# Kernel optimization log

Measured on AMD Instinct MI355X. Metric: run time of the kernel, lower is better.

Reference implementation:

```python
import jax, jax.numpy as jnp
import numpy as np

N_AUTHOR, N_FOS, N_INST, N_PAPER = 100000, 30000, 8000, 200000
D_IN, D_OUT = 128, 128
# (name, n_src, n_dst, n_edges)
RELS = [("aff", N_AUTHOR, N_INST, 150000), ("ita", N_INST, N_AUTHOR, 150000),
        ("writes", N_AUTHOR, N_PAPER, 500000), ("pta", N_PAPER, N_AUTHOR, 500000),
        ("cites", N_PAPER, N_PAPER, 1000000), ("topic", N_PAPER, N_FOS, 500000),
        ("ftp", N_FOS, N_PAPER, 500000)]
NODE_SIZES = {"author": N_AUTHOR, "fos": N_FOS, "inst": N_INST, "paper": N_PAPER}


def setup_inputs() -> dict:
    key = jax.random.key(0)
    ks = iter(jax.random.split(key, 64))
    inp = {}
    for nt, n in NODE_SIZES.items():
        inp[f"x_{nt}"] = jax.random.normal(next(ks), (n, D_IN), jnp.float32)
    for name, ns, nd, e in RELS:
        inp[f"src_{name}"] = jax.random.randint(next(ks), (e,), 0, ns, jnp.int64)
        inp[f"dst_{name}"] = jax.random.randint(next(ks), (e,), 0, nd, jnp.int64)
    w_scale = 1.0 / np.sqrt(D_IN)
    for nt in NODE_SIZES:
        inp[f"W_root_{nt}"] = jax.random.uniform(next(ks), (D_IN, D_OUT), jnp.float32, -w_scale, w_scale)
        inp[f"b_root_{nt}"] = jax.random.uniform(next(ks), (D_OUT,), jnp.float32, -w_scale, w_scale)
    for name, _, _, _ in RELS:
        inp[f"W_{name}"] = jax.random.uniform(next(ks), (D_IN, D_OUT), jnp.float32, -w_scale, w_scale)
    return inp


def _mean_agg(x_src, src, dst, n_dst):
    # gather source features along edges, mean-reduce into destinations
    msg = x_src[src]                                             # [E, D_IN]
    s = jax.ops.segment_sum(msg, dst, num_segments=n_dst)        # [n_dst, D_IN]
    cnt = jax.ops.segment_sum(jnp.ones_like(dst, dtype=x_src.dtype), dst, num_segments=n_dst)
    return s / jnp.maximum(cnt, 1.0)[:, None]                    # isolated nodes -> 0


def reference(x_author, x_fos, x_inst, x_paper,
              W_root_author, b_root_author, W_root_fos, b_root_fos,
              W_root_inst, b_root_inst, W_root_paper, b_root_paper,
              W_aff, W_ita, W_writes, W_pta, W_cites, W_topic, W_ftp,
              src_aff, dst_aff, src_ita, dst_ita, src_writes, dst_writes,
              src_pta, dst_pta, src_cites, dst_cites, src_topic, dst_topic,
              src_ftp, dst_ftp):
    # root (self) transforms
    out_author = x_author @ W_root_author + b_root_author
    out_fos = x_fos @ W_root_fos + b_root_fos
    out_inst = x_inst @ W_root_inst + b_root_inst
    out_paper = x_paper @ W_root_paper + b_root_paper
    # per-relation aggregate -> linear -> accumulate into destination type
    out_inst = out_inst + _mean_agg(x_author, src_aff, dst_aff, N_INST) @ W_aff
    out_author = out_author + _mean_agg(x_inst, src_ita, dst_ita, N_AUTHOR) @ W_ita
    out_paper = out_paper + _mean_agg(x_author, src_writes, dst_writes, N_PAPER) @ W_writes
    out_author = out_author + _mean_agg(x_paper, src_pta, dst_pta, N_AUTHOR) @ W_pta
    out_paper = out_paper + _mean_agg(x_paper, src_cites, dst_cites, N_PAPER) @ W_cites
    out_fos = out_fos + _mean_agg(x_paper, src_topic, dst_topic, N_FOS) @ W_topic
    out_paper = out_paper + _mean_agg(x_fos, src_ftp, dst_ftp, N_PAPER) @ W_ftp
    # concatenate per-type outputs (author, fos, inst, paper) along node axis
    return jnp.concatenate([out_author, out_fos, out_inst, out_paper], axis=0)
```

## Files before the change

### kernel.cpp

```cpp
#include <hip/hip_runtime.h>

#define N_AUTHOR 100000
#define N_FOS    30000
#define N_INST   8000
#define N_PAPER  200000

typedef __attribute__((ext_vector_type(8))) short short8v;
typedef __attribute__((ext_vector_type(4))) float float4v;

__device__ __forceinline__ unsigned short f2bf(float f) {
  unsigned u = __float_as_uint(f);
  u = u + 0x7fffu + ((u >> 16) & 1u);
  return (unsigned short)(u >> 16);
}
#define BF2F(s) __uint_as_float(((unsigned)(unsigned short)(s)) << 16)

__device__ __forceinline__ void acc8(float4v& x, float4v& y, short8v h) {
  x[0] += BF2F(h[0]); x[1] += BF2F(h[1]); x[2] += BF2F(h[2]); x[3] += BF2F(h[3]);
  y[0] += BF2F(h[4]); y[1] += BF2F(h[5]); y[2] += BF2F(h[6]); y[3] += BF2F(h[7]);
}

#define O_CNT    0
#define O_OFFS   3352000
#define O_CURSOR 6704000
#define O_BTOT   10056000
#define O_CSR    10060096
#define O_WT     23260096
#define XB_AUTHOR 23620544
#define XB_FOS    49220544
#define XB_INST   56900544
#define XB_PAPER  58948544
#define WS_NEED_BF 110148544ULL
#define NCNT     838000

struct RelTab { const int* src; const int* dst; int E; int base; };
struct Rels { RelTab r[7]; };
struct WPtrs { const float* w[11]; };
struct XCvt { const float* x; unsigned short* xb; int n8; };

__global__ void prep(WPtrs P, unsigned short* __restrict__ wt,
                     int* __restrict__ cnt, XCvt x0, XCvt x1, XCvt x2, XCvt x3,
                     int doX) {
  int gsz = gridDim.x * blockDim.x;
  int gtid = blockIdx.x * blockDim.x + threadIdx.x;
  for (int i = gtid; i < 11 * 16384; i += gsz) {
    int mat = i >> 14, rem = i & 16383;
    int k = rem >> 7, n = rem & 127;
    wt[mat * 16384 + n * 128 + k] = f2bf(P.w[mat][rem]);
  }
  for (int i = gtid; i < NCNT; i += gsz) cnt[i] = 0;
  if (doX) {
    XCvt xc[4] = {x0, x1, x2, x3};
    #pragma unroll
    for (int a = 0; a < 4; ++a) {
      const float* xp = xc[a].x;
      short8v* xbp = (short8v*)xc[a].xb;
      int n8 = xc[a].n8;
      for (int i = gtid; i < n8; i += gsz) {
        float4v v0 = *(const float4v*)(xp + (size_t)i * 8);
        float4v v1 = *(const float4v*)(xp + (size_t)i * 8 + 4);
        short8v h;
        h[0] = (short)f2bf(v0[0]); h[1] = (short)f2bf(v0[1]);
        h[2] = (short)f2bf(v0[2]); h[3] = (short)f2bf(v0[3]);
        h[4] = (short)f2bf(v1[0]); h[5] = (short)f2bf(v1[1]);
        h[6] = (short)f2bf(v1[2]); h[7] = (short)f2bf(v1[3]);
        xbp[i] = h;
      }
    }
  }
}

__global__ void count_k(Rels R, int* __restrict__ cnt) {
  int gsz = gridDim.x * blockDim.x;
  int gtid = blockIdx.x * blockDim.x + threadIdx.x;
  for (int rr = 0; rr < 7; ++rr) {
    const int* dst = R.r[rr].dst;
    int E = R.r[rr].E, base = R.r[rr].base;
    for (int e = gtid; e < E; e += gsz) atomicAdd(&cnt[base + dst[e]], 1);
  }
}

__global__ void scan1(const int* __restrict__ cnt, int* __restrict__ offs,
                      int* __restrict__ btot, int n) {
  __shared__ int sh[256];
  int tid = threadIdx.x;
  int base = blockIdx.x * 2048 + tid * 8;
  int v[8]; int s = 0;
  #pragma unroll
  for (int i = 0; i < 8; ++i) { v[i] = (base + i < n) ? cnt[base + i] : 0; s += v[i]; }
  sh[tid] = s; __syncthreads();
  for (int off = 1; off < 256; off <<= 1) {
    int t = (tid >= off) ? sh[tid - off] : 0;
    __syncthreads();
    sh[tid] += t;
    __syncthreads();
  }
  int excl = sh[tid] - s;
  if (tid == 255) btot[blockIdx.x] = sh[255];
  int run = excl;
  #pragma unroll
  for (int i = 0; i < 8; ++i) { if (base + i < n) offs[base + i] = run; run += v[i]; }
}

__global__ void scan23(int* __restrict__ offs, int* __restrict__ cursor,
                       const int* __restrict__ btot, int nb, int n) {
  __shared__ int sh[512];
  int tid = threadIdx.x;
  int v = (tid < nb) ? btot[tid] : 0;
  sh[tid] = v; __syncthreads();
  for (int off = 1; off < 512; off <<= 1) {
    int t = (tid >= off) ? sh[tid - off] : 0;
    __syncthreads();
    sh[tid] += t;
    __syncthreads();
  }
  int excl = sh[tid] - v;
  __syncthreads();
  sh[tid] = excl;
  __syncthreads();
  int gsz = gridDim.x * 512;
  for (int idx = blockIdx.x * 512 + tid; idx < n; idx += gsz) {
    int val = offs[idx] + sh[idx >> 11];
    offs[idx] = val;
    cursor[idx] = val;
  }
}

__global__ void fill_k(Rels R, int* __restrict__ cursor, int* __restrict__ csr) {
  int gsz = gridDim.x * blockDim.x;
  int gtid = blockIdx.x * blockDim.x + threadIdx.x;
  for (int rr = 0; rr < 7; ++rr) {
    const int* src = R.r[rr].src;
    const int* dst = R.r[rr].dst;
    int E = R.r[rr].E, base = R.r[rr].base;
    for (int e = gtid; e < E; e += gsz) {
      int p = atomicAdd(&cursor[base + dst[e]], 1);
      csr[p] = src[e];
    }
  }
}

struct GemmSrc { const float* x; const unsigned short* xb;
                 const unsigned short* wt; int cntBase; };
struct TypeArgs {
  GemmSrc s[4];
  int nsrc;
  int bstart;
  int n;
  const float* bias;
  float* out;
};
struct AllArgs {
  TypeArgs t[4];
  const int* offs;
  const int* cnt;
  const int* csr;
};

#define LD4(p) (*(const float4v*)(p))

template <int BF>
__global__ __launch_bounds__(256, 4) void rgcn_gemm(AllArgs A) {
  __shared__ unsigned short a_lds[64 * 128];
  const int tid = threadIdx.x;
  const int wv = tid >> 6, lane = tid & 63;

  int bid = blockIdx.x;
  int ty = (bid >= A.t[3].bstart) ? 3 : (bid >= A.t[2].bstart) ? 2
         : (bid >= A.t[1].bstart) ? 1 : 0;
  const TypeArgs& T = A.t[ty];
  const int rb = (bid - T.bstart) * 64;
  const int n = T.n;

  float4v acc[8];
  #pragma unroll
  for (int i = 0; i < 8; ++i) acc[i] = (float4v)0.0f;

  for (int kb = 0; kb < T.nsrc; ++kb) {
    const GemmSrc S = T.s[kb];
    if (S.cntBase < 0) {
      if (BF) {
        int r = tid >> 2, cb = (tid & 3) * 64;
        int g = rb + r;
        const short8v* p = (const short8v*)(S.xb + (size_t)g * 128 + (cb >> 1));
        #pragma unroll
        for (int k = 0; k < 4; ++k) {
          short8v h = (g < n) ? p[k] : (short8v)0;
          int byte = (r * 256 + cb + k * 16) ^ ((r & 7) << 4);
          *(short8v*)((char*)a_lds + byte) = h;
        }
      } else {
        #pragma unroll
        for (int i = 0; i < 4; ++i) {
          int c = tid + i * 256;
          int r = c >> 4, cc = (c & 15) * 8;
          int g = rb + r;
          short8v hv;
          if (g < n) {
            float4v v0 = LD4(S.x + (size_t)g * 128 + cc);
            float4v v1 = LD4(S.x + (size_t)g * 128 + cc + 4);
            hv[0] = (short)f2bf(v0[0]); hv[1] = (short)f2bf(v0[1]);
            hv[2] = (short)f2bf(v0[2]); hv[3] = (short)f2bf(v0[3]);
            hv[4] = (short)f2bf(v1[0]); hv[5] = (short)f2bf(v1[1]);
            hv[6] = (short)f2bf(v1[2]); hv[7] = (short)f2bf(v1[3]);
          } else hv = (short8v)0;
          int byte = r * 256 + cc * 2; byte ^= (r & 7) << 4;
          *(short8v*)((char*)a_lds + byte) = hv;
        }
      }
    } else if (BF) {
      const int r = tid >> 2;
      const int c0 = (tid & 3) * 32;
      int g = rb + r;
      int gd = S.cntBase + ((g < n) ? g : 0);
      int st = A.offs[gd];
      int deg = (g < n) ? A.cnt[gd] : 0;
      float4v a0 = (float4v)0.f, a1 = (float4v)0.f, a2 = (float4v)0.f,
              a3 = (float4v)0.f, a4 = (float4v)0.f, a5 = (float4v)0.f,
              a6 = (float4v)0.f, a7 = (float4v)0.f;
      int j = 0;
      for (; j + 2 <= deg; j += 2) {
        int i0 = A.csr[st + j], i1 = A.csr[st + j + 1];
        const short8v* p0 = (const short8v*)(S.xb + (size_t)i0 * 128 + c0);
        const short8v* p1 = (const short8v*)(S.xb + (size_t)i1 * 128 + c0);
        short8v h0 = p0[0], h1 = p0[1], h2 = p0[2], h3 = p0[3];
        short8v k0 = p1[0], k1 = p1[1], k2 = p1[2], k3 = p1[3];
        acc8(a0, a1, h0); acc8(a2, a3, h1); acc8(a4, a5, h2); acc8(a6, a7, h3);
        acc8(a0, a1, k0); acc8(a2, a3, k1); acc8(a4, a5, k2); acc8(a6, a7, k3);
      }
      if (j < deg) {
        int i0 = A.csr[st + j];
        const short8v* p0 = (const short8v*)(S.xb + (size_t)i0 * 128 + c0);
        short8v h0 = p0[0], h1 = p0[1], h2 = p0[2], h3 = p0[3];
        acc8(a0, a1, h0); acc8(a2, a3, h1); acc8(a4, a5, h2); acc8(a6, a7, h3);
      }
      float sc = 1.0f / (float)((deg > 0) ? deg : 1);
      a0 *= sc; a1 *= sc; a2 *= sc; a3 *= sc;
      a4 *= sc; a5 *= sc; a6 *= sc; a7 *= sc;
      short8v o0, o1, o2, o3;
      o0[0] = (short)f2bf(a0[0]); o0[1] = (short)f2bf(a0[1]);
      o0[2] = (short)f2bf(a0[2]); o0[3] = (short)f2bf(a0[3]);
      o0[4] = (short)f2bf(a1[0]); o0[5] = (short)f2bf(a1[1]);
      o0[6] = (short)f2bf(a1[2]); o0[7] = (short)f2bf(a1[3]);
      o1[0] = (short)f2bf(a2[0]); o1[1] = (short)f2bf(a2[1]);
      o1[2] = (short)f2bf(a2[2]); o1[3] = (short)f2bf(a2[3]);
      o1[4] = (short)f2bf(a3[0]); o1[5] = (short)f2bf(a3[1]);
      o1[6] = (short)f2bf(a3[2]); o1[7] = (short)f2bf(a3[3]);
      o2[0] = (short)f2bf(a4[0]); o2[1] = (short)f2bf(a4[1]);
      o2[2] = (short)f2bf(a4[2]); o2[3] = (short)f2bf(a4[3]);
      o2[4] = (short)f2bf(a5[0]); o2[5] = (short)f2bf(a5[1]);
      o2[6] = (short)f2bf(a5[2]); o2[7] = (short)f2bf(a5[3]);
      o3[0] = (short)f2bf(a6[0]); o3[1] = (short)f2bf(a6[1]);
      o3[2] = (short)f2bf(a6[2]); o3[3] = (short)f2bf(a6[3]);
      o3[4] = (short)f2bf(a7[0]); o3[5] = (short)f2bf(a7[1]);
      o3[6] = (short)f2bf(a7[2]); o3[7] = (short)f2bf(a7[3]);
      int bbase = r * 256 + c0 * 2;
      int sw = (r & 7) << 4;
      *(short8v*)((char*)a_lds + ((bbase) ^ sw)) = o0;
      *(short8v*)((char*)a_lds + ((bbase + 16) ^ sw)) = o1;
      *(short8v*)((char*)a_lds + ((bbase + 32) ^ sw)) = o2;
      *(short8v*)((char*)a_lds + ((bbase + 48) ^ sw)) = o3;
    } else {
      const int q = lane >> 4;
      const int c0 = (lane & 15) * 8;
      int stA[4], dgA[4];
      #pragma unroll
      for (int rd = 0; rd < 4; ++rd) {
        int r = wv * 16 + rd * 4 + q;
        int g = rb + r;
        int gc = (g < n) ? g : 0;
        int gd = S.cntBase + gc;
        stA[rd] = A.offs[gd];
        dgA[rd] = (g < n) ? A.cnt[gd] : 0;
      }
      #pragma unroll
      for (int rd = 0; rd < 4; ++rd) {
        int r = wv * 16 + rd * 4 + q;
        int st = stA[rd], deg = dgA[rd];
        float a0 = 0.f, a1 = 0.f, a2 = 0.f, a3 = 0.f;
        float a4 = 0.f, a5 = 0.f, a6 = 0.f, a7 = 0.f;
        int j = 0;
        for (; j + 2 <= deg; j += 2) {
          int s0 = A.csr[st + j], s1 = A.csr[st + j + 1];
          const float* p0 = S.x + (size_t)s0 * 128 + c0;
          const float* p1 = S.x + (size_t)s1 * 128 + c0;
          float4v u0 = LD4(p0), u1 = LD4(p0 + 4);
          float4v v0 = LD4(p1), v1 = LD4(p1 + 4);
          a0 += u0[0] + v0[0]; a1 += u0[1] + v0[1];
          a2 += u0[2] + v0[2]; a3 += u0[3] + v0[3];
          a4 += u1[0] + v1[0]; a5 += u1[1] + v1[1];
          a6 += u1[2] + v1[2]; a7 += u1[3] + v1[3];
        }
        if (j < deg) {
          int s0 = A.csr[st + j];
          const float* p0 = S.x + (size_t)s0 * 128 + c0;
          float4v u0 = LD4(p0), u1 = LD4(p0 + 4);
          a0 += u0[0]; a1 += u0[1]; a2 += u0[2]; a3 += u0[3];
          a4 += u1[0]; a5 += u1[1]; a6 += u1[2]; a7 += u1[3];
        }
        float sc = 1.0f / (float)((deg > 0) ? deg : 1);
        short8v hv;
        hv[0] = (short)f2bf(a0 * sc); hv[1] = (short)f2bf(a1 * sc);
        hv[2] = (short)f2bf(a2 * sc); hv[3] = (short)f2bf(a3 * sc);
        hv[4] = (short)f2bf(a4 * sc); hv[5] = (short)f2bf(a5 * sc);
        hv[6] = (short)f2bf(a6 * sc); hv[7] = (short)f2bf(a7 * sc);
        int byte = r * 256 + c0 * 2; byte ^= (r & 7) << 4;
        *(short8v*)((char*)a_lds + byte) = hv;
      }
    }
    __syncthreads();
    short8v af[4];
    #pragma unroll
    for (int ks = 0; ks < 4; ++ks) {
      int r = wv * 16 + (lane & 15);
      int ch = ks * 4 + (lane >> 4);
      int byte = r * 256 + ch * 16; byte ^= (r & 7) << 4;
      af[ks] = *(const short8v*)((const char*)a_lds + byte);
    }
    const unsigned short* wbase = S.wt + (size_t)(lane & 15) * 128
                                + (size_t)(lane >> 4) * 8;
    #pragma unroll
    for (int ct = 0; ct < 8; ++ct) {
      short8v bfr[4];
      #pragma unroll
      for (int ks = 0; ks < 4; ++ks)
        bfr[ks] = *(const short8v*)(wbase + (size_t)ct * 16 * 128 + ks * 32);
      #pragma unroll
      for (int ks = 0; ks < 4; ++ks)
        acc[ct] = __builtin_amdgcn_mfma_f32_16x16x32_bf16(af[ks], bfr[ks], acc[ct], 0, 0, 0);
    }
    __syncthreads();
  }
  #pragma unroll
  for (int ct = 0; ct < 8; ++ct) {
    #pragma unroll
    for (int i = 0; i < 4; ++i) {
      int row = wv * 16 + (lane >> 4) * 4 + i;
      int g = rb + row;
      if (g < n) {
        int col = ct * 16 + (lane & 15);
        T.out[(size_t)g * 128 + col] = acc[ct][i] + T.bias[col];
      }
    }
  }
}

extern "C" void kernel_launch(void* const* d_in, const int* in_sizes, int n_in,
                              void* d_out, int out_size, void* d_ws, size_t ws_size,
                              hipStream_t stream) {
  const float* x_author = (const float*)d_in[0];
  const float* x_fos    = (const float*)d_in[1];
  const float* x_inst   = (const float*)d_in[2];
  const float* x_paper  = (const float*)d_in[3];

  Rels R;
  const int E[7]  = {150000, 150000, 500000, 500000, 1000000, 500000, 500000};
  const int ND[7] = {N_INST, N_AUTHOR, N_PAPER, N_AUTHOR, N_PAPER, N_FOS, N_PAPER};
  int base = 0;
  for (int r = 0; r < 7; ++r) {
    R.r[r].src = (const int*)d_in[4 + 2 * r];
    R.r[r].dst = (const int*)d_in[5 + 2 * r];
    R.r[r].E = E[r];
    R.r[r].base = base;
    base += ND[r];
  }

  char* ws = (char*)d_ws;
  int* cnt    = (int*)(ws + O_CNT);
  int* offs   = (int*)(ws + O_OFFS);
  int* cursor = (int*)(ws + O_CURSOR);
  int* btot   = (int*)(ws + O_BTOT);
  int* csr    = (int*)(ws + O_CSR);
  unsigned short* wt = (unsigned short*)(ws + O_WT);
  unsigned short* xbA = (unsigned short*)(ws + XB_AUTHOR);
  unsigned short* xbF = (unsigned short*)(ws + XB_FOS);
  unsigned short* xbI = (unsigned short*)(ws + XB_INST);
  unsigned short* xbP = (unsigned short*)(ws + XB_PAPER);

  const int useBF = (ws_size >= WS_NEED_BF) ? 1 : 0;

  WPtrs WP;
  WP.w[0] = (const float*)d_in[18];
  WP.w[1] = (const float*)d_in[20];
  WP.w[2] = (const float*)d_in[22];
  WP.w[3] = (const float*)d_in[24];
  for (int r = 0; r < 7; ++r) WP.w[4 + r] = (const float*)d_in[26 + r];

  XCvt xcA = {x_author, xbA, N_AUTHOR * 16};
  XCvt xcF = {x_fos,    xbF, N_FOS * 16};
  XCvt xcI = {x_inst,   xbI, N_INST * 16};
  XCvt xcP = {x_paper,  xbP, N_PAPER * 16};

  prep<<<2048, 256, 0, stream>>>(WP, wt, cnt, xcA, xcF, xcI, xcP, useBF);
  count_k<<<1024, 256, 0, stream>>>(R, cnt);
  scan1<<<410, 256, 0, stream>>>(cnt, offs, btot, NCNT);
  scan23<<<1024, 512, 0, stream>>>(offs, cursor, btot, 410, NCNT);
  fill_k<<<1024, 256, 0, stream>>>(R, cursor, csr);

  float* out = (float*)d_out;
  const int B_AFF = 0, B_ITA = 8000, B_WRITES = 108000, B_PTA = 308000,
            B_CITES = 408000, B_TOPIC = 608000, B_FTP = 638000;

  AllArgs A;
  A.offs = offs; A.cnt = cnt; A.csr = csr;
  for (int t = 0; t < 4; ++t)
    for (int i = 0; i < 4; ++i) A.t[t].s[i] = GemmSrc{nullptr, nullptr, nullptr, 0};

  const int NB_AUTHOR = (N_AUTHOR + 63) / 64;
  const int NB_FOS    = (N_FOS + 63) / 64;
  const int NB_INST   = (N_INST + 63) / 64;
  const int NB_PAPER  = (N_PAPER + 63) / 64;

  A.t[0].s[0] = GemmSrc{x_author, xbA, wt + 0 * 16384, -1};
  A.t[0].s[1] = GemmSrc{x_inst,   xbI, wt + 5 * 16384, B_ITA};
  A.t[0].s[2] = GemmSrc{x_paper,  xbP, wt + 7 * 16384, B_PTA};
  A.t[0].nsrc = 3; A.t[0].bstart = 0; A.t[0].n = N_AUTHOR;
  A.t[0].bias = (const float*)d_in[19]; A.t[0].out = out;

  A.t[1].s[0] = GemmSrc{x_fos,   xbF, wt + 1 * 16384, -1};
  A.t[1].s[1] = GemmSrc{x_paper, xbP, wt + 9 * 16384, B_TOPIC};
  A.t[1].nsrc = 2; A.t[1].bstart = NB_AUTHOR; A.t[1].n = N_FOS;
  A.t[1].bias = (const float*)d_in[21]; A.t[1].out = out + (size_t)100000 * 128;

  A.t[2].s[0] = GemmSrc{x_inst,   xbI, wt + 2 * 16384, -1};
  A.t[2].s[1] = GemmSrc{x_author, xbA, wt + 4 * 16384, B_AFF};
  A.t[2].nsrc = 2; A.t[2].bstart = NB_AUTHOR + NB_FOS; A.t[2].n = N_INST;
  A.t[2].bias = (const float*)d_in[23]; A.t[2].out = out + (size_t)130000 * 128;

  A.t[3].s[0] = GemmSrc{x_paper,  xbP, wt + 3 * 16384, -1};
  A.t[3].s[1] = GemmSrc{x_author, xbA, wt + 6 * 16384, B_WRITES};
  A.t[3].s[2] = GemmSrc{x_paper,  xbP, wt + 8 * 16384, B_CITES};
  A.t[3].s[3] = GemmSrc{x_fos,    xbF, wt + 10 * 16384, B_FTP};
  A.t[3].nsrc = 4; A.t[3].bstart = NB_AUTHOR + NB_FOS + NB_INST; A.t[3].n = N_PAPER;
  A.t[3].bias = (const float*)d_in[25]; A.t[3].out = out + (size_t)138000 * 128;

  const int NB_TOTAL = NB_AUTHOR + NB_FOS + NB_INST + NB_PAPER;
  if (useBF)
    rgcn_gemm<1><<<NB_TOTAL, 256, 0, stream>>>(A);
  else
    rgcn_gemm<0><<<NB_TOTAL, 256, 0, stream>>>(A);
}
```

Measured before the change: 900.3 us.

## Split aggregation into separate gather kernel and feed bf16 aggregates to MFMA GEMM

```diff
diff --git a/kernel.cpp b/kernel.cpp
--- a/kernel.cpp
+++ b/kernel.cpp
@@ -30,7 +30,9 @@
 #define XB_FOS    49220544
 #define XB_INST   56900544
 #define XB_PAPER  58948544
-#define WS_NEED_BF 110148544ULL
+#define O_AGG     110148544
+#define WS_NEED_BF  110148544ULL
+#define WS_NEED_AGG 324676544ULL
 #define NCNT     838000
 
 struct RelTab { const int* src; const int* dst; int E; int base; };
@@ -140,13 +142,115 @@
   }
 }
 
+struct AggArgs {
+  const unsigned short* xb[7];
+  const int* offs; const int* cnt; const int* csr;
+  unsigned short* agg;
+};
+
+__global__ __launch_bounds__(256, 8) void agg_k(AggArgs G) {
+  const int w = blockIdx.x * 4 + (threadIdx.x >> 6);
+  const int lane = threadIdx.x & 63;
+  int rel = (w >= 638000) ? 6 : (w >= 608000) ? 5 : (w >= 408000) ? 4
+          : (w >= 308000) ? 3 : (w >= 108000) ? 2 : (w >= 8000) ? 1 : 0;
+  const unsigned short* xb = G.xb[rel];
+  const int st = G.offs[w];
+  const int deg = G.cnt[w];
+  const int ce = lane * 2;
+  float a0 = 0.f, a1 = 0.f;
+  for (int j = 0; j < deg; j += 8) {
+    int rem = deg - j;
+    int nb = (rem > 8) ? 8 : rem;
+    int vidx = 0;
+    if (lane < nb) vidx = G.csr[st + j + lane];
+    unsigned r0 = 0, r1 = 0, r2 = 0, r3 = 0, r4 = 0, r5 = 0, r6 = 0, r7 = 0;
+    int s;
+    if (nb > 0) { s = __builtin_amdgcn_readlane(vidx, 0); r0 = *(const unsigned*)(xb + (size_t)s * 128 + ce); }
+    if (nb > 1) { s = __builtin_amdgcn_readlane(vidx, 1); r1 = *(const unsigned*)(xb + (size_t)s * 128 + ce); }
+    if (nb > 2) { s = __builtin_amdgcn_readlane(vidx, 2); r2 = *(const unsigned*)(xb + (size_t)s * 128 + ce); }
+    if (nb > 3) { s = __builtin_amdgcn_readlane(vidx, 3); r3 = *(const unsigned*)(xb + (size_t)s * 128 + ce); }
+    if (nb > 4) { s = __builtin_amdgcn_readlane(vidx, 4); r4 = *(const unsigned*)(xb + (size_t)s * 128 + ce); }
+    if (nb > 5) { s = __builtin_amdgcn_readlane(vidx, 5); r5 = *(const unsigned*)(xb + (size_t)s * 128 + ce); }
+    if (nb > 6) { s = __builtin_amdgcn_readlane(vidx, 6); r6 = *(const unsigned*)(xb + (size_t)s * 128 + ce); }
+    if (nb > 7) { s = __builtin_amdgcn_readlane(vidx, 7); r7 = *(const unsigned*)(xb + (size_t)s * 128 + ce); }
+    if (nb > 0) { a0 += __uint_as_float(r0 << 16); a1 += __uint_as_float(r0 & 0xffff0000u); }
+    if (nb > 1) { a0 += __uint_as_float(r1 << 16); a1 += __uint_as_float(r1 & 0xffff0000u); }
+    if (nb > 2) { a0 += __uint_as_float(r2 << 16); a1 += __uint_as_float(r2 & 0xffff0000u); }
+    if (nb > 3) { a0 += __uint_as_float(r3 << 16); a1 += __uint_as_float(r3 & 0xffff0000u); }
+    if (nb > 4) { a0 += __uint_as_float(r4 << 16); a1 += __uint_as_float(r4 & 0xffff0000u); }
+    if (nb > 5) { a0 += __uint_as_float(r5 << 16); a1 += __uint_as_float(r5 & 0xffff0000u); }
+    if (nb > 6) { a0 += __uint_as_float(r6 << 16); a1 += __uint_as_float(r6 & 0xffff0000u); }
+    if (nb > 7) { a0 += __uint_as_float(r7 << 16); a1 += __uint_as_float(r7 & 0xffff0000u); }
+  }
+  float sc = 1.0f / (float)((deg > 0) ? deg : 1);
+  unsigned h0 = f2bf(a0 * sc), h1 = f2bf(a1 * sc);
+  *(unsigned*)(G.agg + (size_t)w * 128 + ce) = h0 | (h1 << 16);
+}
+
+struct Type2 {
+  const unsigned short* src[4];
+  const unsigned short* wtp[4];
+  int nsrc, bstart, n;
+  const float* bias;
+  float* out;
+};
+struct All2 { Type2 t[4]; };
+
+__global__ __launch_bounds__(256, 4) void rgcn_gemm_agg(All2 A) {
+  const int tid = threadIdx.x;
+  const int wv = tid >> 6, lane = tid & 63;
+  int bid = blockIdx.x;
+  int ty = (bid >= A.t[3].bstart) ? 3 : (bid >= A.t[2].bstart) ? 2
+         : (bid >= A.t[1].bstart) ? 1 : 0;
+  const Type2& T = A.t[ty];
+  const int rb = (bid - T.bstart) * 64;
+  const int n = T.n;
+
+  int ar = rb + wv * 16 + (lane & 15);
+  if (ar >= n) ar = n - 1;
+  const int ach = lane >> 4;
+
+  float4v acc[8];
+  #pragma unroll
+  for (int i = 0; i < 8; ++i) acc[i] = (float4v)0.0f;
+
+  for (int kb = 0; kb < T.nsrc; ++kb) {
+    const unsigned short* abase = T.src[kb] + (size_t)ar * 128 + ach * 8;
+    short8v af[4];
+    #pragma unroll
+    for (int ks = 0; ks < 4; ++ks)
+      af[ks] = *(const short8v*)(abase + ks * 32);
+    const unsigned short* wbase = T.wtp[kb] + (size_t)(lane & 15) * 128 + ach * 8;
+    #pragma unroll
+    for (int ct = 0; ct < 8; ++ct) {
+      short8v bfr[4];
+      #pragma unroll
+      for (int ks = 0; ks < 4; ++ks)
+        bfr[ks] = *(const short8v*)(wbase + (size_t)ct * 2048 + ks * 32);
+      #pragma unroll
+      for (int ks = 0; ks < 4; ++ks)
+        acc[ct] = __builtin_amdgcn_mfma_f32_16x16x32_bf16(af[ks], bfr[ks], acc[ct], 0, 0, 0);
+    }
+  }
+  #pragma unroll
+  for (int ct = 0; ct < 8; ++ct) {
+    #pragma unroll
+    for (int i = 0; i < 4; ++i) {
+      int row = wv * 16 + (lane >> 4) * 4 + i;
+      int g = rb + row;
+      if (g < n) {
+        int col = ct * 16 + (lane & 15);
+        T.out[(size_t)g * 128 + col] = acc[ct][i] + T.bias[col];
+      }
+    }
+  }
+}
+
 struct GemmSrc { const float* x; const unsigned short* xb;
                  const unsigned short* wt; int cntBase; };
 struct TypeArgs {
   GemmSrc s[4];
-  int nsrc;
-  int bstart;
-  int n;
+  int nsrc, bstart, n;
   const float* bias;
   float* out;
 };
@@ -376,8 +480,10 @@
   unsigned short* xbF = (unsigned short*)(ws + XB_FOS);
   unsigned short* xbI = (unsigned short*)(ws + XB_INST);
   unsigned short* xbP = (unsigned short*)(ws + XB_PAPER);
-
-  const int useBF = (ws_size >= WS_NEED_BF) ? 1 : 0;
+  unsigned short* agg = (unsigned short*)(ws + O_AGG);
+
+  const int useBF  = (ws_size >= WS_NEED_BF) ? 1 : 0;
+  const int useAGG = (ws_size >= WS_NEED_AGG) ? 1 : 0;
 
   WPtrs WP;
   WP.w[0] = (const float*)d_in[18];
@@ -392,51 +498,88 @@
   XCvt xcP = {x_paper,  xbP, N_PAPER * 16};
 
   prep<<<2048, 256, 0, stream>>>(WP, wt, cnt, xcA, xcF, xcI, xcP, useBF);
-  count_k<<<1024, 256, 0, stream>>>(R, cnt);
+  count_k<<<2048, 256, 0, stream>>>(R, cnt);
   scan1<<<410, 256, 0, stream>>>(cnt, offs, btot, NCNT);
   scan23<<<1024, 512, 0, stream>>>(offs, cursor, btot, 410, NCNT);
-  fill_k<<<1024, 256, 0, stream>>>(R, cursor, csr);
+  fill_k<<<2048, 256, 0, stream>>>(R, cursor, csr);
 
   float* out = (float*)d_out;
   const int B_AFF = 0, B_ITA = 8000, B_WRITES = 108000, B_PTA = 308000,
             B_CITES = 408000, B_TOPIC = 608000, B_FTP = 638000;
-
-  AllArgs A;
-  A.offs = offs; A.cnt = cnt; A.csr = csr;
-  for (int t = 0; t < 4; ++t)
-    for (int i = 0; i < 4; ++i) A.t[t].s[i] = GemmSrc{nullptr, nullptr, nullptr, 0};
 
   const int NB_AUTHOR = (N_AUTHOR + 63) / 64;
   const int NB_FOS    = (N_FOS + 63) / 64;
   const int NB_INST   = (N_INST + 63) / 64;
   const int NB_PAPER  = (N_PAPER + 63) / 64;
-
-  A.t[0].s[0] = GemmSrc{x_author, xbA, wt + 0 * 16384, -1};
-  A.t[0].s[1] = GemmSrc{x_inst,   xbI, wt + 5 * 16384, B_ITA};
-  A.t[0].s[2] = GemmSrc{x_paper,  xbP, wt + 7 * 16384, B_PTA};
-  A.t[0].nsrc = 3; A.t[0].bstart = 0; A.t[0].n = N_AUTHOR;
-  A.t[0].bias = (const float*)d_in[19]; A.t[0].out = out;
-
-  A.t[1].s[0] = GemmSrc{x_fos,   xbF, wt + 1 * 16384, -1};
-  A.t[1].s[1] = GemmSrc{x_paper, xbP, wt + 9 * 16384, B_TOPIC};
-  A.t[1].nsrc = 2; A.t[1].bstart = NB_AUTHOR; A.t[1].n = N_FOS;
-  A.t[1].bias = (const float*)d_in[21]; A.t[1].out = out + (size_t)100000 * 128;
-
-  A.t[2].s[0] = GemmSrc{x_inst,   xbI, wt + 2 * 16384, -1};
-  A.t[2].s[1] = GemmSrc{x_author, xbA, wt + 4 * 16384, B_AFF};
-  A.t[2].nsrc = 2; A.t[2].bstart = NB_AUTHOR + NB_FOS; A.t[2].n = N_INST;
-  A.t[2].bias = (const float*)d_in[23]; A.t[2].out = out + (size_t)130000 * 128;
-
-  A.t[3].s[0] = GemmSrc{x_paper,  xbP, wt + 3 * 16384, -1};
-  A.t[3].s[1] = GemmSrc{x_author, xbA, wt + 6 * 16384, B_WRITES};
-  A.t[3].s[2] = GemmSrc{x_paper,  xbP, wt + 8 * 16384, B_CITES};
-  A.t[3].s[3] = GemmSrc{x_fos,    xbF, wt + 10 * 16384, B_FTP};
-  A.t[3].nsrc = 4; A.t[3].bstart = NB_AUTHOR + NB_FOS + NB_INST; A.t[3].n = N_PAPER;
-  A.t[3].bias = (const float*)d_in[25]; A.t[3].out = out + (size_t)138000 * 128;
-
   const int NB_TOTAL = NB_AUTHOR + NB_FOS + NB_INST + NB_PAPER;
-  if (useBF)
-    rgcn_gemm<1><<<NB_TOTAL, 256, 0, stream>>>(A);
-  else
-    rgcn_gemm<0><<<NB_TOTAL, 256, 0, stream>>>(A);
-}
+
+  if (useAGG) {
+    AggArgs GA;
+    GA.xb[0] = xbA; GA.xb[1] = xbI; GA.xb[2] = xbA; GA.xb[3] = xbP;
+    GA.xb[4] = xbP; GA.xb[5] = xbP; GA.xb[6] = xbF;
+    GA.offs = offs; GA.cnt = cnt; GA.csr = csr; GA.agg = agg;
+    agg_k<<<NCNT / 4, 256, 0, stream>>>(GA);
+
+    All2 A2;
+    for (int t = 0; t < 4; ++t)
+      for (int i = 0; i < 4; ++i) { A2.t[t].src[i] = nullptr; A2.t[t].wtp[i] = nullptr; }
+
+    A2.t[0].src[0] = xbA;                        A2.t[0].wtp[0] = wt + 0 * 16384;
+    A2.t[0].src[1] = agg + (size_t)B_ITA * 128;  A2.t[0].wtp[1] = wt + 5 * 16384;
+    A2.t[0].src[2] = agg + (size_t)B_PTA * 128;  A2.t[0].wtp[2] = wt + 7 * 16384;
+    A2.t[0].nsrc = 3; A2.t[0].bstart = 0; A2.t[0].n = N_AUTHOR;
+    A2.t[0].bias = (const float*)d_in[19]; A2.t[0].out = out;
+
+    A2.t[1].src[0] = xbF;                          A2.t[1].wtp[0] = wt + 1 * 16384;
+    A2.t[1].src[1] = agg + (size_t)B_TOPIC * 128;  A2.t[1].wtp[1] = wt + 9 * 16384;
+    A2.t[1].nsrc = 2; A2.t[1].bstart = NB_AUTHOR; A2.t[1].n = N_FOS;
+    A2.t[1].bias = (const float*)d_in[21]; A2.t[1].out = out + (size_t)100000 * 128;
+
+    A2.t[2].src[0] = xbI;                        A2.t[2].wtp[0] = wt + 2 * 16384;
+    A2.t[2].src[1] = agg + (size_t)B_AFF * 128;  A2.t[2].wtp[1] = wt + 4 * 16384;
+    A2.t[2].nsrc = 2; A2.t[2].bstart = NB_AUTHOR + NB_FOS; A2.t[2].n = N_INST;
+    A2.t[2].bias = (const float*)d_in[23]; A2.t[2].out = out + (size_t)130000 * 128;
+
+    A2.t[3].src[0] = xbP;                           A2.t[3].wtp[0] = wt + 3 * 16384;
+    A2.t[3].src[1] = agg + (size_t)B_WRITES * 128;  A2.t[3].wtp[1] = wt + 6 * 16384;
+    A2.t[3].src[2] = agg + (size_t)B_CITES * 128;   A2.t[3].wtp[2] = wt + 8 * 16384;
+    A2.t[3].src[3] = agg + (size_t)B_FTP * 128;     A2.t[3].wtp[3] = wt + 10 * 16384;
+    A2.t[3].nsrc = 4; A2.t[3].bstart = NB_AUTHOR + NB_FOS + NB_INST; A2.t[3].n = N_PAPER;
+    A2.t[3].bias = (const float*)d_in[25]; A2.t[3].out = out + (size_t)138000 * 128;
+
+    rgcn_gemm_agg<<<NB_TOTAL, 256, 0, stream>>>(A2);
+  } else {
+    AllArgs A;
+    A.offs = offs; A.cnt = cnt; A.csr = csr;
+    for (int t = 0; t < 4; ++t)
+      for (int i = 0; i < 4; ++i) A.t[t].s[i] = GemmSrc{nullptr, nullptr, nullptr, 0};
+
+    A.t[0].s[0] = GemmSrc{x_author, xbA, wt + 0 * 16384, -1};
+    A.t[0].s[1] = GemmSrc{x_inst,   xbI, wt + 5 * 16384, B_ITA};
+    A.t[0].s[2] = GemmSrc{x_paper,  xbP, wt + 7 * 16384, B_PTA};
+    A.t[0].nsrc = 3; A.t[0].bstart = 0; A.t[0].n = N_AUTHOR;
+    A.t[0].bias = (const float*)d_in[19]; A.t[0].out = out;
+
+    A.t[1].s[0] = GemmSrc{x_fos,   xbF, wt + 1 * 16384, -1};
+    A.t[1].s[1] = GemmSrc{x_paper, xbP, wt + 9 * 16384, B_TOPIC};
+    A.t[1].nsrc = 2; A.t[1].bstart = NB_AUTHOR; A.t[1].n = N_FOS;
+    A.t[1].bias = (const float*)d_in[21]; A.t[1].out = out + (size_t)100000 * 128;
+
+    A.t[2].s[0] = GemmSrc{x_inst,   xbI, wt + 2 * 16384, -1};
+    A.t[2].s[1] = GemmSrc{x_author, xbA, wt + 4 * 16384, B_AFF};
+    A.t[2].nsrc = 2; A.t[2].bstart = NB_AUTHOR + NB_FOS; A.t[2].n = N_INST;
+    A.t[2].bias = (const float*)d_in[23]; A.t[2].out = out + (size_t)130000 * 128;
+
+    A.t[3].s[0] = GemmSrc{x_paper,  xbP, wt + 3 * 16384, -1};
+    A.t[3].s[1] = GemmSrc{x_author, xbA, wt + 6 * 16384, B_WRITES};
+    A.t[3].s[2] = GemmSrc{x_paper,  xbP, wt + 8 * 16384, B_CITES};
+    A.t[3].s[3] = GemmSrc{x_fos,    xbF, wt + 10 * 16384, B_FTP};
+    A.t[3].nsrc = 4; A.t[3].bstart = NB_AUTHOR + NB_FOS + NB_INST; A.t[3].n = N_PAPER;
+    A.t[3].bias = (const float*)d_in[25]; A.t[3].out = out + (size_t)138000 * 128;
+
+    if (useBF)
+      rgcn_gemm<1><<<NB_TOTAL, 256, 0, stream>>>(A);
+    else
+      rgcn_gemm<0><<<NB_TOTAL, 256, 0, stream>>>(A);
+  }
+}
```

After: 1.074 ms. +19.3%, slower.
